# Optimization experiments

Hardware: AMD Instinct MI355X
Metric: run time of the kernel (lower is better)

Reference implementation:

```python
import jax, jax.numpy as jnp
import numpy as np

SHIFT = 1e-09  # input_shift


def _patches(v, kh, kw):
    # v: (B, C, H, W) -> (B, C, kh*kw, Ho, Wo), VALID padding, stride 1
    B, C, H, W = v.shape
    Ho, Wo = H - kh + 1, W - kw + 1
    cols = [v[:, :, i:i + Ho, j:j + Wo] for i in range(kh) for j in range(kw)]
    return jnp.stack(cols, axis=2)


def setup_inputs() -> dict:
    key = jax.random.key(0)
    kx, k1k, k2k, kb = jax.random.split(key, 4)
    B, C, H, W = 32, 64, 64, 64
    kh, kw, F = 3, 3, 128
    x = jax.random.normal(kx, (B, C, H, W), dtype=jnp.float32)
    # log-domain kernels (learned params of the two Add modules)
    k1 = jax.random.normal(k1k, (kh, kw, C, F), dtype=jnp.float32) * 0.1
    k2 = jax.random.normal(k2k, (kh, kw, C, F), dtype=jnp.float32) * 0.1
    bias = jnp.zeros((F,), dtype=jnp.float32)
    return {"x": x, "k1": k1, "k2": k2, "bias": bias}


def reference(x, k1, k2, bias):
    kh, kw, C, F = k1.shape
    # Ln: log of ReLU'd patches (positive and negative parts of x)
    ep_pos = jnp.exp(jnp.log(jax.nn.relu(_patches(x, kh, kw)) + SHIFT))   # (B,C,kh*kw,Ho,Wo)
    ep_neg = jnp.exp(jnp.log(jax.nn.relu(_patches(-x, kh, kw)) + SHIFT))
    # Add + Exp + patch reduction: sum_p exp(ln_patch + k) == einsum(exp(ln_patch), exp(k))
    ek1 = jnp.exp(k1).reshape(kh * kw, C, F)
    ek2 = jnp.exp(k2).reshape(kh * kw, C, F)
    y11 = jnp.einsum('bckhw,kcf->bfhw', ep_pos, ek1)
    y12 = jnp.einsum('bckhw,kcf->bfhw', ep_pos, ek2)
    y21 = jnp.einsum('bckhw,kcf->bfhw', ep_neg, ek1)
    y22 = jnp.einsum('bckhw,kcf->bfhw', ep_neg, ek2)
    return y11 - y12 - y21 + y22 + bias[None, :, None, None]
```

## Files before the change

### kernel.cpp

```cpp
#include <hip/hip_runtime.h>
#include <hip/hip_bf16.h>

typedef __attribute__((ext_vector_type(4))) float f32x4;
typedef __attribute__((ext_vector_type(8))) short bf16x8;

static __device__ __forceinline__ unsigned int f2bf(float f) {
    unsigned int u = __float_as_uint(f);
    return (u + 0x7FFFu + ((u >> 16) & 1u)) >> 16;
}

static __device__ __forceinline__ void gload_lds16(const void* g, void* l) {
    __builtin_amdgcn_global_load_lds(
        (const __attribute__((address_space(1))) unsigned int*)g,
        (__attribute__((address_space(3))) unsigned int*)l, 16, 0, 0);
}

__global__ __launch_bounds__(256) void wprep_kernel(const float* __restrict__ k1,
                                                    const float* __restrict__ k2,
                                                    unsigned short* __restrict__ wq) {
    int idx = blockIdx.x * 256 + threadIdx.x;
    if (idx >= 73728) return;
    int f  = idx & 127;
    int ch = (idx >> 7) & 31;
    int kh = (idx >> 12) & 1;
    int p  = idx >> 13;
    int src = (p * 64 + kh * 32 + ch) * 128 + f;
    float v = expf(k1[src]) - expf(k2[src]);
    wq[((p * 2 + kh) * 128 + f) * 32 + ch] = (unsigned short)f2bf(v);
}

__global__ __launch_bounds__(256) void xprep_kernel(const float* __restrict__ x,
                                                    unsigned short* __restrict__ xsw) {
    __shared__ float t[64][65];
    int b = blockIdx.x >> 6;
    int h = blockIdx.x & 63;
    const float* xb = x + b * 262144 + h * 64;
    int tid = threadIdx.x;
    int col4 = (tid & 15) * 4;
    int c0   = tid >> 4;
#pragma unroll
    for (int i = 0; i < 4; ++i) {
        int c = c0 + i * 16;
        f32x4 v = *(const f32x4*)(xb + c * 4096 + col4);
        t[c][col4 + 0] = v[0]; t[c][col4 + 1] = v[1];
        t[c][col4 + 2] = v[2]; t[c][col4 + 3] = v[3];
    }
    __syncthreads();
    unsigned short* orow = xsw + ((b * 64 + h) * 64) * 64;
#pragma unroll
    for (int i = 0; i < 2; ++i) {
        int j   = tid + i * 256;
        int col = j >> 3;
        int cb  = ((j & 7) ^ (col & 7)) * 8;
        uint4 pk;
        pk.x = f2bf(t[cb + 0][col]) | (f2bf(t[cb + 1][col]) << 16);
        pk.y = f2bf(t[cb + 2][col]) | (f2bf(t[cb + 3][col]) << 16);
        pk.z = f2bf(t[cb + 4][col]) | (f2bf(t[cb + 5][col]) << 16);
        pk.w = f2bf(t[cb + 6][col]) | (f2bf(t[cb + 7][col]) << 16);
        *(uint4*)(orow + j * 8) = pk;
    }
}

__global__ __launch_bounds__(256, 2) void conv_kernel(const unsigned short* __restrict__ xsw,
                                                      const unsigned short* __restrict__ wq,
                                                      const float* __restrict__ bias,
                                                      float* __restrict__ out) {
    __shared__ unsigned short xs[4 * 64 * 64];

    int bid0 = blockIdx.x;
    int bid  = (bid0 & 7) * 124 + (bid0 >> 3);
    int b    = bid / 31;
    int tile = bid - b * 31;
    int oh0  = tile * 2;

    int tid  = threadIdx.x;
    int lane = tid & 63;
    int wid  = tid >> 6;
    int wr   = wid >> 1;
    int wc   = wid & 1;
    int lr   = lane & 15;
    int hi   = lane >> 4;

    {
        const char* src = (const char*)(xsw + ((b * 64 + oh0) * 64) * 64);
        char* dst = (char*)xs;
#pragma unroll
        for (int i = 0; i < 8; ++i) {
            int chunk = (i * 4 + wid) * 1024;
            gload_lds16(src + chunk + lane * 16, dst + chunk);
        }
    }

    const bf16x8* wg = (const bf16x8*)wq;
    int fb0 = wc * 64 + lr;
    bf16x8 wfrag[2][8];
#pragma unroll
    for (int kh = 0; kh < 2; ++kh)
#pragma unroll
        for (int ni = 0; ni < 4; ++ni)
            wfrag[0][kh * 4 + ni] = wg[(kh * 128 + fb0 + ni * 16) * 4 + hi];

    f32x4 acc[4][4];
#pragma unroll
    for (int ni = 0; ni < 4; ++ni)
#pragma unroll
        for (int mi = 0; mi < 4; ++mi) acc[ni][mi] = (f32x4){0.f, 0.f, 0.f, 0.f};

    __syncthreads();

#pragma unroll
    for (int p = 0; p < 9; ++p) {
        const int cur = p & 1, nxt = cur ^ 1;
        if (p < 8) {
#pragma unroll
            for (int kh = 0; kh < 2; ++kh)
#pragma unroll
                for (int ni = 0; ni < 4; ++ni)
                    wfrag[nxt][kh * 4 + ni] = wg[(((p + 1) * 2 + kh) * 128 + fb0 + ni * 16) * 4 + hi];
        }
        const int ki = p / 3, kj = p % 3;
#pragma unroll
        for (int kb = 0; kb < 2; ++kb) {
            int c0 = kb * 32 + hi * 8;
            bf16x8 af[4];
#pragma unroll
            for (int mi = 0; mi < 4; ++mi) {
                int col  = mi * 16 + lr + kj;
                int colc = col > 63 ? 63 : col;
                af[mi] = *(const bf16x8*)(&xs[(((wr + ki) * 64 + colc) << 6) + (c0 ^ ((colc & 7) << 3))]);
            }
#pragma unroll
            for (int ni = 0; ni < 4; ++ni)
#pragma unroll
                for (int mi = 0; mi < 4; ++mi)
                    acc[ni][mi] = __builtin_amdgcn_mfma_f32_16x16x32_bf16(
                        wfrag[cur][kb * 4 + ni], af[mi], acc[ni][mi], 0, 0, 0);
        }
    }

    int oh = oh0 + wr;
    float* ob = out + b * (128 * 62 * 62);
#pragma unroll
    for (int ni = 0; ni < 4; ++ni) {
        int fb = wc * 64 + ni * 16 + (hi << 2);
        f32x4 bv4 = *(const f32x4*)(bias + fb);
#pragma unroll
        for (int t = 0; t < 4; ++t) {
            float* orow = ob + ((fb + t) * 62 + oh) * 62;
#pragma unroll
            for (int mi = 0; mi < 4; ++mi) {
                int ow = mi * 16 + lr;
                if (ow < 62) orow[ow] = acc[ni][mi][t] + bv4[t];
            }
        }
    }
}

extern "C" void kernel_launch(void* const* d_in, const int* in_sizes, int n_in,
                              void* d_out, int out_size, void* d_ws, size_t ws_size,
                              hipStream_t stream) {
    const float* x    = (const float*)d_in[0];
    const float* k1   = (const float*)d_in[1];
    const float* k2   = (const float*)d_in[2];
    const float* bias = (const float*)d_in[3];
    float* out = (float*)d_out;

    unsigned short* wq  = (unsigned short*)d_ws;
    unsigned short* xsw = (unsigned short*)d_ws + 73728;

    hipLaunchKernelGGL(wprep_kernel, dim3(288), dim3(256), 0, stream, k1, k2, wq);
    hipLaunchKernelGGL(xprep_kernel, dim3(2048), dim3(256), 0, stream, x, xsw);
    hipLaunchKernelGGL(conv_kernel, dim3(992), dim3(256), 0, stream, x  == nullptr ? xsw : xsw, wq, bias, out);
}
```

Before: 136.3 us.

## Stage swizzled weights in LDS with double buffering and enlarge output row tile

New measurement: 118.3 us. 13.2% less time.

```diff
diff --git a/kernel.cpp b/kernel.cpp
--- a/kernel.cpp
+++ b/kernel.cpp
@@ -18,15 +18,22 @@
 __global__ __launch_bounds__(256) void wprep_kernel(const float* __restrict__ k1,
                                                     const float* __restrict__ k2,
                                                     unsigned short* __restrict__ wq) {
-    int idx = blockIdx.x * 256 + threadIdx.x;
-    if (idx >= 73728) return;
-    int f  = idx & 127;
-    int ch = (idx >> 7) & 31;
-    int kh = (idx >> 12) & 1;
-    int p  = idx >> 13;
-    int src = (p * 64 + kh * 32 + ch) * 128 + f;
-    float v = expf(k1[src]) - expf(k2[src]);
-    wq[((p * 2 + kh) * 128 + f) * 32 + ch] = (unsigned short)f2bf(v);
+    int g = blockIdx.x * 256 + threadIdx.x;
+    if (g >= 9216) return;
+    int cc = g & 7;
+    int f  = (g >> 3) & 127;
+    int p  = g >> 10;
+    unsigned int w[4];
+#pragma unroll
+    for (int e2 = 0; e2 < 4; ++e2) {
+        int s0 = (p * 64 + cc * 8 + e2 * 2) * 128 + f;
+        unsigned int lo = f2bf(expf(k1[s0]) - expf(k2[s0]));
+        int s1 = s0 + 128;
+        unsigned int hh = f2bf(expf(k1[s1]) - expf(k2[s1]));
+        w[e2] = lo | (hh << 16);
+    }
+    *(uint4*)(wq + p * 8192 + f * 64 + ((cc * 8) ^ ((f & 7) << 3))) =
+        *(const uint4*)w;
 }
 
 __global__ __launch_bounds__(256) void xprep_kernel(const float* __restrict__ x,
@@ -46,7 +53,7 @@
         t[c][col4 + 2] = v[2]; t[c][col4 + 3] = v[3];
     }
     __syncthreads();
-    unsigned short* orow = xsw + ((b * 64 + h) * 64) * 64;
+    unsigned short* orow = xsw + ((size_t)(b * 64 + h)) * 4096;
 #pragma unroll
     for (int i = 0; i < 2; ++i) {
         int j   = tid + i * 256;
@@ -65,13 +72,14 @@
                                                       const unsigned short* __restrict__ wq,
                                                       const float* __restrict__ bias,
                                                       float* __restrict__ out) {
-    __shared__ unsigned short xs[4 * 64 * 64];
+    __shared__ unsigned short xs[6 * 64 * 64];
+    __shared__ unsigned short bs[2][128 * 64];
 
     int bid0 = blockIdx.x;
-    int bid  = (bid0 & 7) * 124 + (bid0 >> 3);
-    int b    = bid / 31;
-    int tile = bid - b * 31;
-    int oh0  = tile * 2;
+    int bid  = (bid0 & 7) * 64 + (bid0 >> 3);
+    int b    = bid >> 4;
+    int tile = bid & 15;
+    int oh0  = tile * 4;
 
     int tid  = threadIdx.x;
     int lane = tid & 63;
@@ -82,75 +90,88 @@
     int hi   = lane >> 4;
 
     {
-        const char* src = (const char*)(xsw + ((b * 64 + oh0) * 64) * 64);
-        char* dst = (char*)xs;
+        const unsigned short* srcb = xsw + (size_t)b * 262144;
 #pragma unroll
-        for (int i = 0; i < 8; ++i) {
-            int chunk = (i * 4 + wid) * 1024;
-            gload_lds16(src + chunk + lane * 16, dst + chunk);
+        for (int i = 0; i < 12; ++i) {
+            int chunk = i * 4 + wid;
+            int row   = chunk >> 3;
+            int srow  = oh0 + row; if (srow > 63) srow = 63;
+            gload_lds16((const char*)(srcb + srow * 4096) + (chunk & 7) * 1024 + lane * 16,
+                        (char*)xs + chunk * 1024);
+        }
+#pragma unroll
+        for (int i = 0; i < 4; ++i) {
+            int chunk = i * 4 + wid;
+            gload_lds16((const char*)wq + chunk * 1024 + lane * 16,
+                        (char*)bs[0] + chunk * 1024);
         }
     }
 
-    const bf16x8* wg = (const bf16x8*)wq;
-    int fb0 = wc * 64 + lr;
-    bf16x8 wfrag[2][8];
-#pragma unroll
-    for (int kh = 0; kh < 2; ++kh)
-#pragma unroll
-        for (int ni = 0; ni < 4; ++ni)
-            wfrag[0][kh * 4 + ni] = wg[(kh * 128 + fb0 + ni * 16) * 4 + hi];
-
-    f32x4 acc[4][4];
+    f32x4 acc[4][8];
 #pragma unroll
     for (int ni = 0; ni < 4; ++ni)
 #pragma unroll
-        for (int mi = 0; mi < 4; ++mi) acc[ni][mi] = (f32x4){0.f, 0.f, 0.f, 0.f};
-
-    __syncthreads();
+        for (int q = 0; q < 8; ++q) acc[ni][q] = (f32x4){0.f, 0.f, 0.f, 0.f};
 
 #pragma unroll
     for (int p = 0; p < 9; ++p) {
-        const int cur = p & 1, nxt = cur ^ 1;
+        asm volatile("s_waitcnt vmcnt(0)" ::: "memory");
+        __builtin_amdgcn_s_barrier();
+        __builtin_amdgcn_sched_barrier(0);
         if (p < 8) {
 #pragma unroll
-            for (int kh = 0; kh < 2; ++kh)
-#pragma unroll
-                for (int ni = 0; ni < 4; ++ni)
-                    wfrag[nxt][kh * 4 + ni] = wg[(((p + 1) * 2 + kh) * 128 + fb0 + ni * 16) * 4 + hi];
+            for (int i = 0; i < 4; ++i) {
+                int chunk = i * 4 + wid;
+                gload_lds16((const char*)wq + (p + 1) * 16384 + chunk * 1024 + lane * 16,
+                            (char*)bs[(p + 1) & 1] + chunk * 1024);
+            }
         }
         const int ki = p / 3, kj = p % 3;
+        const unsigned short* bc = bs[p & 1];
 #pragma unroll
         for (int kb = 0; kb < 2; ++kb) {
             int c0 = kb * 32 + hi * 8;
-            bf16x8 af[4];
+            bf16x8 bfr[4];
 #pragma unroll
-            for (int mi = 0; mi < 4; ++mi) {
-                int col  = mi * 16 + lr + kj;
-                int colc = col > 63 ? 63 : col;
-                af[mi] = *(const bf16x8*)(&xs[(((wr + ki) * 64 + colc) << 6) + (c0 ^ ((colc & 7) << 3))]);
+            for (int ni = 0; ni < 4; ++ni) {
+                int f = wc * 64 + ni * 16 + lr;
+                bfr[ni] = *(const bf16x8*)(&bc[f * 64 + (c0 ^ ((f & 7) << 3))]);
             }
 #pragma unroll
-            for (int ni = 0; ni < 4; ++ni)
+            for (int oh2 = 0; oh2 < 2; ++oh2) {
+                int row = wr * 2 + oh2 + ki;
 #pragma unroll
-                for (int mi = 0; mi < 4; ++mi)
-                    acc[ni][mi] = __builtin_amdgcn_mfma_f32_16x16x32_bf16(
-                        wfrag[cur][kb * 4 + ni], af[mi], acc[ni][mi], 0, 0, 0);
+                for (int mi = 0; mi < 4; ++mi) {
+                    int col  = mi * 16 + lr + kj;
+                    int colc = col > 63 ? 63 : col;
+                    bf16x8 af = *(const bf16x8*)(&xs[((row * 64 + colc) << 6) + (c0 ^ ((colc & 7) << 3))]);
+#pragma unroll
+                    for (int ni = 0; ni < 4; ++ni)
+                        acc[ni][oh2 * 4 + mi] = __builtin_amdgcn_mfma_f32_16x16x32_bf16(
+                            bfr[ni], af, acc[ni][oh2 * 4 + mi], 0, 0, 0);
+                }
+            }
         }
     }
 
-    int oh = oh0 + wr;
-    float* ob = out + b * (128 * 62 * 62);
+    float* ob = out + b * 492032;
 #pragma unroll
     for (int ni = 0; ni < 4; ++ni) {
         int fb = wc * 64 + ni * 16 + (hi << 2);
         f32x4 bv4 = *(const f32x4*)(bias + fb);
 #pragma unroll
         for (int t = 0; t < 4; ++t) {
-            float* orow = ob + ((fb + t) * 62 + oh) * 62;
 #pragma unroll
-            for (int mi = 0; mi < 4; ++mi) {
-                int ow = mi * 16 + lr;
-                if (ow < 62) orow[ow] = acc[ni][mi][t] + bv4[t];
+            for (int oh2 = 0; oh2 < 2; ++oh2) {
+                int oh = oh0 + wr * 2 + oh2;
+                if (oh < 62) {
+                    float* orow = ob + ((fb + t) * 62 + oh) * 62;
+#pragma unroll
+                    for (int mi = 0; mi < 4; ++mi) {
+                        int ow = mi * 16 + lr;
+                        if (ow < 62) orow[ow] = acc[ni][oh2 * 4 + mi][t] + bv4[t];
+                    }
+                }
             }
         }
     }
@@ -168,7 +189,7 @@
     unsigned short* wq  = (unsigned short*)d_ws;
     unsigned short* xsw = (unsigned short*)d_ws + 73728;
 
-    hipLaunchKernelGGL(wprep_kernel, dim3(288), dim3(256), 0, stream, k1, k2, wq);
+    hipLaunchKernelGGL(wprep_kernel, dim3(36), dim3(256), 0, stream, k1, k2, wq);
     hipLaunchKernelGGL(xprep_kernel, dim3(2048), dim3(256), 0, stream, x, xsw);
-    hipLaunchKernelGGL(conv_kernel, dim3(992), dim3(256), 0, stream, x  == nullptr ? xsw : xsw, wq, bias, out);
+    hipLaunchKernelGGL(conv_kernel, dim3(512), dim3(256), 0, stream, xsw, wq, bias, out);
 }
```
